# Performance work log

Hardware: AMD Instinct MI355X
Metric: run time of the kernel (lower is better)

## Reference

```python
import jax, jax.numpy as jnp
import numpy as np

FACTOR = 1.0
KERNEL = 3
PAD = 1
STRIDE = 1


def setup_inputs() -> dict:
    key = jax.random.key(0)
    ks = jax.random.split(key, 7)
    B_, Cin, Cout, L, CODE = 32, 128, 128, 4096, 2
    return {
        "input": jax.random.normal(ks[0], (B_, Cin, L), dtype=jnp.float32),
        "codes": jax.random.normal(ks[1], (B_, CODE, CODE), dtype=jnp.float32),
        "weight": jax.random.normal(ks[2], (Cout, Cin, KERNEL), dtype=jnp.float32) * 0.05,
        "A": jax.random.normal(ks[3], (Cin, CODE, KERNEL), dtype=jnp.float32) * 0.05,
        "B": jax.random.normal(ks[4], (Cout, CODE, KERNEL), dtype=jnp.float32) * 0.05,
        "bias": jax.random.normal(ks[5], (Cout,), dtype=jnp.float32) * 0.05,
        "bias_context": jax.random.normal(ks[6], (CODE, Cout), dtype=jnp.float32) * 0.05,
    }


def reference(input, codes, weight, A, B, bias, bias_context):
    # Hypernetwork-generated per-sample conv weights (low-rank via codes)
    w = jnp.einsum('ick,bcr->birk', A, codes)            # (b, in, code, k)
    context_w = jnp.einsum('birk,ork->boik', w, B)       # (b, out, in, k)
    combined_weight = weight + FACTOR * context_w        # (b, out, in, k)

    diag = jnp.diagonal(codes, axis1=-2, axis2=-1)       # (b, code)
    context_bias = diag @ bias_context                   # (b, out)
    combined_bias = bias + FACTOR * context_bias         # (b, out)

    # circular padding along spatial axis
    padded = jnp.pad(input, ((0, 0), (0, 0), (PAD, PAD)), mode='wrap')
    L_out = (input.shape[-1] + 2 * PAD - KERNEL) // STRIDE + 1
    # windowed view: (b, in, L_out, k) via k shifted slices (k is tiny, loop ok)
    windows = jnp.stack([padded[:, :, j:j + L_out * STRIDE:STRIDE] for j in range(KERNEL)], axis=-1)
    out = jnp.einsum('bihw,boiw->boh', windows, combined_weight)
    return out + combined_bias[..., None]
```

## Files before the change

kernel.cpp:

```cpp
#include <hip/hip_runtime.h>
#include <hip/hip_bf16.h>
#include <stdint.h>
#include <stddef.h>

#define L_LEN 4096
#define CIN   128
#define COUT  128
#define NB    32
#define KTOT  384
#define TN    64
#define TPB   4
#define ROWS  (TN + 2)

typedef __bf16 bf16x8 __attribute__((ext_vector_type(8)));
typedef float  f32x4  __attribute__((ext_vector_type(4)));

__device__ __forceinline__ uint16_t f2bf(float f) {
    union { float f; uint32_t u; } v; v.f = f;
    return (uint16_t)((v.u + 0x7fffu + ((v.u >> 16) & 1u)) >> 16);
}
__device__ __forceinline__ uint32_t pack2(float lo, float hi) {
    return (uint32_t)f2bf(lo) | ((uint32_t)f2bf(hi) << 16);
}

__global__ __launch_bounds__(256) void geps_combine(
    const float* __restrict__ codes, const float* __restrict__ weight,
    const float* __restrict__ Amat,  const float* __restrict__ Bmat,
    const float* __restrict__ bias,  const float* __restrict__ bias_ctx,
    uint16_t* __restrict__ Wc, float* __restrict__ cbias)
{
    int tid = blockIdx.x * 256 + threadIdx.x;
    if (tid < NB * COUT * KTOT) {
        int j    = tid & 7;
        int lane = (tid >> 3) & 63;
        int mt   = (tid >> 9) & 1;
        int tmp  = tid >> 10;
        int t    = tmp % 12;
        int bo   = tmp / 12;
        int og   = bo & 3;
        int b    = bo >> 2;
        int col  = t * 32 + (lane >> 4) * 8 + j;
        int k    = col >> 7;
        int i    = col & 127;
        int o    = og * 32 + mt * 16 + (lane & 15);
        float cw = 0.f;
        #pragma unroll
        for (int c = 0; c < 2; ++c) {
            float a = Amat[i * 6 + c * 3 + k];
            #pragma unroll
            for (int r = 0; r < 2; ++r)
                cw += a * codes[b * 4 + c * 2 + r] * Bmat[o * 6 + r * 3 + k];
        }
        float val = weight[o * 384 + i * 3 + k] + cw;
        Wc[tid] = f2bf(val);
    }
    if (tid < NB * COUT) {
        int b = tid >> 7, o = tid & 127;
        float cb = bias[o];
        #pragma unroll
        for (int c = 0; c < 2; ++c)
            cb += codes[b * 4 + c * 2 + c] * bias_ctx[c * 128 + o];
        cbias[tid] = cb;
    }
}


#define LOAD_HALF(IT, H0)                                                    \
    {                                                                        \
        int L_p4 = ((IT) << 4) + (tid >> 4);                                 \
        int L_qd = tid & 15;                                                 \
        const float* L_r0 = inb + (size_t)(4 * L_p4) * L_LEN + (H0) + 4 * L_qd; \
        st[0] = *(const float4*)(L_r0);                                      \
        st[1] = *(const float4*)(L_r0 + L_LEN);                              \
        st[2] = *(const float4*)(L_r0 + 2 * L_LEN);                          \
        st[3] = *(const float4*)(L_r0 + 3 * L_LEN);                          \
        if ((IT) && tid < 128) {                                             \
            int L_p    = tid & 63;                                           \
            int L_side = tid >> 6;                                           \
            int L_r    = L_side ? (ROWS - 1) : 0;                            \
            int L_gh   = ((H0) - 1 + L_r) & (L_LEN - 1);                     \
            hx0 = inb[(size_t)(2 * L_p) * L_LEN + L_gh];                     \
            hx1 = inb[(size_t)(2 * L_p + 1) * L_LEN + L_gh];                 \
        }                                                                    \
    }

#define PACK_HALF(IT, XP)                                                    \
    {                                                                        \
        uint16_t* P_Xw = (XP);                                               \
        int P_p4 = ((IT) << 4) + (tid >> 4);                                 \
        int P_qd = tid & 15;                                                 \
        const int P_off = (4 * P_p4) & 7;                                    \
        const int P_pc  = P_p4 >> 1;                                         \
        _Pragma("unroll")                                                    \
        for (int P_j4 = 0; P_j4 < 4; ++P_j4) {                               \
            int P_r  = 1 + 4 * P_qd + P_j4;                                  \
            int P_ch = P_pc ^ (P_r & 15);                                    \
            uint2 P_w;                                                       \
            P_w.x = pack2(((const float*)&st[0])[P_j4],                      \
                          ((const float*)&st[1])[P_j4]);                     \
            P_w.y = pack2(((const float*)&st[2])[P_j4],                      \
                          ((const float*)&st[3])[P_j4]);                     \
            *(uint2*)&P_Xw[P_r * 128 + (P_ch << 3) + P_off] = P_w;           \
        }                                                                    \
        if ((IT) && tid < 128) {                                             \
            int P_p     = tid & 63;                                          \
            int P_side  = tid >> 6;                                          \
            int P_hr    = P_side ? (ROWS - 1) : 0;                           \
            int P_chunk = (P_p >> 2) ^ (P_hr & 15);                          \
            *(uint32_t*)&P_Xw[P_hr * 128 + (P_chunk << 3) + ((2 * P_p) & 7)] = \
                pack2(hx0, hx1);                                             \
        }                                                                    \
    }

#define KHALF(T0, XR)                                                        \
    {                                                                        \
        const uint16_t* K_X = (XR);                                          \
        bf16x8 K_a0 = *(const bf16x8*)(WcW + (T0) * 1024);                   \
        bf16x8 K_a1 = *(const bf16x8*)(WcW + (T0) * 1024 + 512);             \
        _Pragma("unroll")                                                    \
        for (int K_tt = 0; K_tt < 6; ++K_tt) {                               \
            const int K_t  = (T0) + K_tt;                                    \
            const int K_tn = (K_t + 1 < 12) ? (K_t + 1) : 11;                \
            bf16x8 K_n0 = *(const bf16x8*)(WcW + K_tn * 1024);               \
            bf16x8 K_n1 = *(const bf16x8*)(WcW + K_tn * 1024 + 512);         \
            const int K_k   = K_t >> 2;                                      \
            const int K_i0c = (K_t & 3) << 2;                                \
            bf16x8 K_bfv[4];                                                 \
            _Pragma("unroll")                                                \
            for (int K_nt = 0; K_nt < 4; ++K_nt) {                           \
                int K_r  = K_nt * 16 + m16 + K_k;                            \
                int K_ch = (K_i0c + q) ^ (K_r & 15);                         \
                K_bfv[K_nt] = *(const bf16x8*)&K_X[K_r * 128 + (K_ch << 3)]; \
            }                                                                \
            _Pragma("unroll")                                                \
            for (int K_nt = 0; K_nt < 4; ++K_nt) {                           \
                acc[0][K_nt] = __builtin_amdgcn_mfma_f32_16x16x32_bf16(      \
                    K_a0, K_bfv[K_nt], acc[0][K_nt], 0, 0, 0);               \
                acc[1][K_nt] = __builtin_amdgcn_mfma_f32_16x16x32_bf16(      \
                    K_a1, K_bfv[K_nt], acc[1][K_nt], 0, 0, 0);               \
            }                                                                \
            K_a0 = K_n0; K_a1 = K_n1;                                        \
        }                                                                    \
    }

__global__ __launch_bounds__(256, 2) void geps_conv(
    const float* __restrict__ in, const uint16_t* __restrict__ Wc,
    const float* __restrict__ cbias, float* __restrict__ out)
{
    __shared__ uint16_t __attribute__((aligned(16))) Xt[2][ROWS * 128];
    __shared__ float cb[COUT];

    const int tid  = threadIdx.x;
    const int b    = blockIdx.y;
    const int hb   = blockIdx.x * (TN * TPB);
    const int lane = tid & 63;
    const int wid  = tid >> 6;
    const int m16  = lane & 15;
    const int q    = lane >> 4;
    const int mq   = wid * 32;

    if (tid < COUT) cb[tid] = cbias[b * COUT + tid];

    const float* inb = in + (size_t)b * CIN * L_LEN;
    const uint16_t* WcW = Wc + (size_t)(b * 4 + wid) * 12288 + lane * 8;

    float4 st[4];
    float  hx0 = 0.f, hx1 = 0.f;
    f32x4  acc[2][4];

    LOAD_HALF(0, hb)
    PACK_HALF(0, &Xt[0][0])
    LOAD_HALF(1, hb)
    PACK_HALF(1, &Xt[0][0])
    __syncthreads();

    #pragma unroll 1
    for (int j = 0; j < TPB; ++j) {
        const int h0 = hb + j * TN;
        uint16_t* Xcur = &Xt[j & 1][0];
        uint16_t* Xnxt = &Xt[(j + 1) & 1][0];
        const bool pre = (j + 1 < TPB);

        if (pre) LOAD_HALF(0, h0 + TN)
        asm volatile("" ::: "memory");

        #pragma unroll
        for (int a = 0; a < 2; ++a)
            #pragma unroll
            for (int c = 0; c < 4; ++c) acc[a][c] = 0.0f;

        KHALF(0, Xcur)

        if (pre) {
            PACK_HALF(0, Xnxt)
            LOAD_HALF(1, h0 + TN)
            asm volatile("" ::: "memory");
        }

        KHALF(6, Xcur)

        float* outb = out + (size_t)b * COUT * L_LEN + h0;
        #pragma unroll
        for (int mt = 0; mt < 2; ++mt) {
            #pragma unroll
            for (int reg = 0; reg < 4; ++reg) {
                int o = mq + mt * 16 + q * 4 + reg;
                float bv = cb[o];
                float* orow = outb + (size_t)o * L_LEN;
                #pragma unroll
                for (int nt = 0; nt < 4; ++nt)
                    __builtin_nontemporal_store(acc[mt][nt][reg] + bv,
                                                &orow[nt * 16 + m16]);
            }
        }

        if (pre) PACK_HALF(1, Xnxt)
        __syncthreads();
    }
}

extern "C" void kernel_launch(void* const* d_in, const int* in_sizes, int n_in,
                              void* d_out, int out_size, void* d_ws, size_t ws_size,
                              hipStream_t stream) {
    const float* input    = (const float*)d_in[0];
    const float* codes    = (const float*)d_in[1];
    const float* weight   = (const float*)d_in[2];
    const float* Amat     = (const float*)d_in[3];
    const float* Bmat     = (const float*)d_in[4];
    const float* bias     = (const float*)d_in[5];
    const float* bias_ctx = (const float*)d_in[6];
    float* out = (float*)d_out;

    uint16_t* Wc    = (uint16_t*)d_ws;
    float*    cbias = (float*)((char*)d_ws + (size_t)NB * COUT * KTOT * 2);

    geps_combine<<<dim3((NB * COUT * KTOT) / 256), 256, 0, stream>>>(
        codes, weight, Amat, Bmat, bias, bias_ctx, Wc, cbias);
    geps_conv<<<dim3(L_LEN / (TN * TPB), NB), 256, 0, stream>>>(
        input, Wc, cbias, out);
}
```

Before: 147.9 us.

## Prefetch weight fragments two steps ahead and remap blocks to a 1D grid

The two six-step KHALF macro invocations become a single 12-step unrolled loop that keeps a three-slot register ring of A fragments, loading weights two steps ahead instead of one. This is meant to hide global/L2 latency on weight loads behind more MFMAs. The grid becomes 1D with a custom block-to-(batch, tile) mapping that interleaves batches across consecutive block IDs, likely to spread weight and input reads across XCDs/L2 slices. The cost is extra VGPRs for the deeper prefetch, which could hurt occupancy under launch_bounds(256,2).

```diff
diff --git a/kernel.cpp b/kernel.cpp
--- a/kernel.cpp
+++ b/kernel.cpp
@@ -112,37 +112,6 @@
         }                                                                    \
     }
 
-#define KHALF(T0, XR)                                                        \
-    {                                                                        \
-        const uint16_t* K_X = (XR);                                          \
-        bf16x8 K_a0 = *(const bf16x8*)(WcW + (T0) * 1024);                   \
-        bf16x8 K_a1 = *(const bf16x8*)(WcW + (T0) * 1024 + 512);             \
-        _Pragma("unroll")                                                    \
-        for (int K_tt = 0; K_tt < 6; ++K_tt) {                               \
-            const int K_t  = (T0) + K_tt;                                    \
-            const int K_tn = (K_t + 1 < 12) ? (K_t + 1) : 11;                \
-            bf16x8 K_n0 = *(const bf16x8*)(WcW + K_tn * 1024);               \
-            bf16x8 K_n1 = *(const bf16x8*)(WcW + K_tn * 1024 + 512);         \
-            const int K_k   = K_t >> 2;                                      \
-            const int K_i0c = (K_t & 3) << 2;                                \
-            bf16x8 K_bfv[4];                                                 \
-            _Pragma("unroll")                                                \
-            for (int K_nt = 0; K_nt < 4; ++K_nt) {                           \
-                int K_r  = K_nt * 16 + m16 + K_k;                            \
-                int K_ch = (K_i0c + q) ^ (K_r & 15);                         \
-                K_bfv[K_nt] = *(const bf16x8*)&K_X[K_r * 128 + (K_ch << 3)]; \
-            }                                                                \
-            _Pragma("unroll")                                                \
-            for (int K_nt = 0; K_nt < 4; ++K_nt) {                           \
-                acc[0][K_nt] = __builtin_amdgcn_mfma_f32_16x16x32_bf16(      \
-                    K_a0, K_bfv[K_nt], acc[0][K_nt], 0, 0, 0);               \
-                acc[1][K_nt] = __builtin_amdgcn_mfma_f32_16x16x32_bf16(      \
-                    K_a1, K_bfv[K_nt], acc[1][K_nt], 0, 0, 0);               \
-            }                                                                \
-            K_a0 = K_n0; K_a1 = K_n1;                                        \
-        }                                                                    \
-    }
-
 __global__ __launch_bounds__(256, 2) void geps_conv(
     const float* __restrict__ in, const uint16_t* __restrict__ Wc,
     const float* __restrict__ cbias, float* __restrict__ out)
@@ -151,8 +120,9 @@
     __shared__ float cb[COUT];
 
     const int tid  = threadIdx.x;
-    const int b    = blockIdx.y;
-    const int hb   = blockIdx.x * (TN * TPB);
+    const int d    = blockIdx.x;
+    const int b    = 4 * (d & 7) + (d >> 7);
+    const int hb   = ((d >> 3) & 15) * (TN * TPB);
     const int lane = tid & 63;
     const int wid  = tid >> 6;
     const int m16  = lane & 15;
@@ -189,15 +159,40 @@
             #pragma unroll
             for (int c = 0; c < 4; ++c) acc[a][c] = 0.0f;
 
-        KHALF(0, Xcur)
-
-        if (pre) {
-            PACK_HALF(0, Xnxt)
-            LOAD_HALF(1, h0 + TN)
-            asm volatile("" ::: "memory");
+        bf16x8 ar[3][2];
+        ar[0][0] = *(const bf16x8*)(WcW);
+        ar[0][1] = *(const bf16x8*)(WcW + 512);
+        ar[1][0] = *(const bf16x8*)(WcW + 1024);
+        ar[1][1] = *(const bf16x8*)(WcW + 1536);
+
+        #pragma unroll
+        for (int t = 0; t < 12; ++t) {
+            if (t + 2 < 12) {
+                ar[(t + 2) % 3][0] = *(const bf16x8*)(WcW + (t + 2) * 1024);
+                ar[(t + 2) % 3][1] = *(const bf16x8*)(WcW + (t + 2) * 1024 + 512);
+            }
+            if (t == 6 && pre) {
+                PACK_HALF(0, Xnxt)
+                LOAD_HALF(1, h0 + TN)
+                asm volatile("" ::: "memory");
+            }
+            const int k   = t >> 2;
+            const int i0c = (t & 3) << 2;
+            bf16x8 bfv[4];
+            #pragma unroll
+            for (int nt = 0; nt < 4; ++nt) {
+                int r  = nt * 16 + m16 + k;
+                int ch = (i0c + q) ^ (r & 15);
+                bfv[nt] = *(const bf16x8*)&Xcur[r * 128 + (ch << 3)];
+            }
+            #pragma unroll
+            for (int nt = 0; nt < 4; ++nt) {
+                acc[0][nt] = __builtin_amdgcn_mfma_f32_16x16x32_bf16(
+                    ar[t % 3][0], bfv[nt], acc[0][nt], 0, 0, 0);
+                acc[1][nt] = __builtin_amdgcn_mfma_f32_16x16x32_bf16(
+                    ar[t % 3][1], bfv[nt], acc[1][nt], 0, 0, 0);
+            }
         }
-
-        KHALF(6, Xcur)
 
         float* outb = out + (size_t)b * COUT * L_LEN + h0;
         #pragma unroll
@@ -236,6 +231,6 @@
 
     geps_combine<<<dim3((NB * COUT * KTOT) / 256), 256, 0, stream>>>(
         codes, weight, Amat, Bmat, bias, bias_ctx, Wc, cbias);
-    geps_conv<<<dim3(L_LEN / (TN * TPB), NB), 256, 0, stream>>>(
+    geps_conv<<<dim3(NB * L_LEN / (TN * TPB)), 256, 0, stream>>>(
         input, Wc, cbias, out);
 }
```

After: 144.8 us. -2.1%, faster.
